# Kernel tuning notes

Measured on AMD Instinct MI355X. Metric: run time of the kernel, lower is better.

The kernel has to match this reference:

```python
import jax, jax.numpy as jnp
import numpy as np

B, T, C, H = 4, 2048, 1024, 16
D = C // H  # head dim = 64


def setup_inputs() -> dict:
    key = jax.random.key(0)
    ks = jax.random.split(key, 5)
    s = 1.0 / np.sqrt(C)
    return {
        "x": jax.random.normal(ks[0], (B, T, C), dtype=jnp.float32),
        "Wq": jax.random.normal(ks[1], (C, C), dtype=jnp.float32) * s,
        "bq": jnp.zeros((C,), dtype=jnp.float32),
        "Wk": jax.random.normal(ks[2], (C, C), dtype=jnp.float32) * s,
        "bk": jnp.zeros((C,), dtype=jnp.float32),
        "Wv": jax.random.normal(ks[3], (C, C), dtype=jnp.float32) * s,
        "bv": jnp.zeros((C,), dtype=jnp.float32),
        "Wp": jax.random.normal(ks[4], (C, C), dtype=jnp.float32) * s,
        "bp": jnp.zeros((C,), dtype=jnp.float32),
    }


def reference(x, Wq, bq, Wk, bk, Wv, bv, Wp, bp):
    Bb, Tt, Cc = x.shape
    # QKV projections (torch Linear: y = x @ W.T + b)
    q = (x @ Wq.T + bq).reshape(Bb, Tt, H, D).transpose(0, 2, 1, 3)  # [B,H,T,D]
    k = (x @ Wk.T + bk).reshape(Bb, Tt, H, D).transpose(0, 2, 1, 3)
    v = (x @ Wv.T + bv).reshape(Bb, Tt, H, D).transpose(0, 2, 1, 3)
    att = jnp.einsum("bhqd,bhkd->bhqk", q, k) / jnp.sqrt(jnp.float32(D))
    causal = jnp.tril(jnp.ones((Tt, Tt), dtype=bool))
    att = jnp.where(causal[None, None], att, -jnp.inf)
    att = jax.nn.softmax(att, axis=-1)
    y = jnp.einsum("bhqk,bhkd->bhqd", att, v)  # [B,H,T,D]
    y = y.transpose(0, 2, 1, 3).reshape(Bb, Tt, Cc)
    return y @ Wp.T + bp
```

## Files before the change

### kernel.cpp

```cpp
#include <hip/hip_runtime.h>

typedef unsigned short u16;
typedef unsigned int u32;

typedef __attribute__((ext_vector_type(4))) float f32x4;
typedef __attribute__((ext_vector_type(8))) short bf16x8;


__device__ inline u16 f2b(float f) {
  union { float f; u32 u; } x; x.f = f;
  u32 u = x.u;
  u32 r = (u + 0x7fffu + ((u >> 16) & 1u)) >> 16;
  return (u16)r;
}

__device__ inline u32 cvtpk(float lo, float hi) {
  u32 r;
  asm("v_cvt_pk_bf16_f32 %0, %1, %2" : "=v"(r) : "v"(lo), "v"(hi));
  return r;
}

__device__ inline void gload_lds16(const void* g, void* l) {
  __builtin_amdgcn_global_load_lds(
      (const __attribute__((address_space(1))) u32*)g,
      (__attribute__((address_space(3))) u32*)l, 16, 0, 0);
}


__global__ __launch_bounds__(256) void cvt_all(const float* __restrict__ x,
                                               const float* __restrict__ w0,
                                               const float* __restrict__ w1,
                                               const float* __restrict__ w2,
                                               const float* __restrict__ w3,
                                               u16* __restrict__ xs,
                                               u16* __restrict__ wsz,
                                               u16* __restrict__ wp) {
  int b = blockIdx.x, t = threadIdx.x;
  const float* src;
  char* dst;
  if (b < 5632) {
    int g = b * 256 + t;
    int row;
    if (b < 4096) {
      row = g >> 7;
      src = x + (size_t)row * 1024;
      dst = (char*)xs;
    } else {
      g -= 1048576;
      row = g >> 7;
      src = (row < 1024) ? w0 + (size_t)row * 1024
           : (row < 2048) ? w1 + (size_t)(row - 1024) * 1024
                          : w2 + (size_t)(row - 2048) * 1024;
      dst = (char*)wsz;
    }
    int c = g & 127;
    int kt = c >> 3, cc = (c & 7) ^ (row & 7);
    float4 lo = *(const float4*)(src + c * 8);
    float4 hi = *(const float4*)(src + c * 8 + 4);
    union { u16 s[8]; uint4 v; } o;
    o.s[0] = f2b(lo.x); o.s[1] = f2b(lo.y); o.s[2] = f2b(lo.z); o.s[3] = f2b(lo.w);
    o.s[4] = f2b(hi.x); o.s[5] = f2b(hi.y); o.s[6] = f2b(hi.z); o.s[7] = f2b(hi.w);
    *(uint4*)(dst + (size_t)(row >> 8) * 524288 + kt * 32768 +
              (row & 255) * 128 + cc * 16) = o.v;
  } else {
    int g = (b - 5632) * 256 + t;
    float4 lo = *(const float4*)(w3 + (size_t)g * 8);
    float4 hi = *(const float4*)(w3 + (size_t)g * 8 + 4);
    union { u16 s[8]; uint4 v; } o;
    o.s[0] = f2b(lo.x); o.s[1] = f2b(lo.y); o.s[2] = f2b(lo.z); o.s[3] = f2b(lo.w);
    o.s[4] = f2b(hi.x); o.s[5] = f2b(hi.y); o.s[6] = f2b(hi.z); o.s[7] = f2b(hi.w);
    *(uint4*)((char*)wp + (size_t)g * 16) = o.v;
  }
}


__global__ __launch_bounds__(512) void gemm_qkv(const u16* __restrict__ Aswz,
                                                const u16* __restrict__ Wswz,
                                                const float* __restrict__ bq,
                                                const float* __restrict__ bk,
                                                const float* __restrict__ bv,
                                                u16* __restrict__ outQ,
                                                u16* __restrict__ outK,
                                                u16* __restrict__ outVt,
                                                float qscale) {
  __shared__ u16 lds[3][24576];

  const int t = threadIdx.x;
  const int lane = t & 63;
  const int w = t >> 6;
  const int wm = w >> 1, wn = w & 1;
  const int lr = lane & 15, lg = lane >> 4;

  int bid = blockIdx.y * 24 + blockIdx.x;
  int swz = (bid & 7) * 96 + (bid >> 3);
  const int mBase = (swz / 24) * 256;
  const int nBase = (swz % 24) * 128;
  const int mode = nBase >> 10;
  const int noff = nBase & 255;

  const char* Ap = (const char*)Aswz + (size_t)(mBase >> 8) * 524288;
  const char* Bp = (const char*)Wswz + (size_t)(nBase >> 8) * 524288 +
                   noff * 128;

  f32x4 acc[4][4];
#pragma unroll
  for (int i = 0; i < 4; ++i)
#pragma unroll
    for (int j = 0; j < 4; ++j) acc[i][j] = (f32x4){0.f, 0.f, 0.f, 0.f};

  auto stage = [&](int buf, int kt2) {
    const char* As = Ap + (size_t)kt2 * 32768;
    const char* Bs = Bp + (size_t)kt2 * 32768;
    char* Ad = (char*)&lds[buf][0];
    char* Bd = (char*)&lds[buf][16384];
#pragma unroll
    for (int l = 0; l < 4; ++l)
      gload_lds16(As + (l * 512 + t) * 16, Ad + (l * 512 + t) * 16);
#pragma unroll
    for (int l = 0; l < 2; ++l)
      gload_lds16(Bs + (l * 512 + t) * 16, Bd + (l * 512 + t) * 16);
  };

  stage(0, 0);
  stage(1, 1);

  for (int kt = 0; kt < 16; ++kt) {
    if (kt < 15) asm volatile("s_waitcnt vmcnt(6)" ::: "memory");
    else         asm volatile("s_waitcnt vmcnt(0)" ::: "memory");
    __builtin_amdgcn_s_barrier();
    if (kt + 2 < 16) stage((kt + 2) % 3, kt + 2);

    const int cb = kt % 3;
    const char* Ab = (const char*)&lds[cb][0];
    const char* Bb = (const char*)&lds[cb][16384];

    bf16x8 af[4][2], bf[4][2];
#pragma unroll
    for (int i = 0; i < 4; ++i) {
      int row = wm * 64 + i * 16 + lr;
#pragma unroll
      for (int kk = 0; kk < 2; ++kk)
        af[i][kk] = *(const bf16x8*)(Ab + row * 128 +
                                     ((kk * 64 + lg * 16) ^ ((row & 7) << 4)));
    }
#pragma unroll
    for (int j = 0; j < 4; ++j) {
      int rn = wn * 64 + j * 16 + lr;
#pragma unroll
      for (int kk = 0; kk < 2; ++kk)
        bf[j][kk] = *(const bf16x8*)(Bb + rn * 128 +
                                     ((kk * 64 + lg * 16) ^ ((rn & 7) << 4)));
    }

    __builtin_amdgcn_s_setprio(1);
#pragma unroll
    for (int i = 0; i < 4; ++i)
#pragma unroll
      for (int j = 0; j < 4; ++j)
#pragma unroll
        for (int kk = 0; kk < 2; ++kk)
          acc[i][j] = __builtin_amdgcn_mfma_f32_16x16x32_bf16(
              af[i][kk], bf[j][kk], acc[i][j], 0, 0, 0);
    __builtin_amdgcn_s_setprio(0);
  }

#pragma unroll
  for (int i = 0; i < 4; ++i) {
    int row = mBase + wm * 64 + i * 16 + lg * 4;
    int b_ = row >> 11, tp = row & 2047;
#pragma unroll
    for (int j = 0; j < 4; ++j) {
      int col = nBase + wn * 64 + j * 16 + lr;
      int ncol = col & 1023;
      int h = ncol >> 6, dd = ncol & 63;
      size_t bhOff = (size_t)(b_ * 16 + h) * 262144;
      if (mode == 2) {
        float bv_ = bv[ncol];
        ushort4 o;
        o.x = f2b(acc[i][j][0] + bv_);
        o.y = f2b(acc[i][j][1] + bv_);
        o.z = f2b(acc[i][j][2] + bv_);
        o.w = f2b(acc[i][j][3] + bv_);
        *(ushort4*)((char*)outVt + bhOff + (tp >> 6) * 8192 + dd * 128 +
                    ((((tp & 63) >> 3) << 4) ^ ((dd & 7) << 4)) +
                    (tp & 7) * 2) = o;
      } else if (mode == 0) {
        float bv_ = bq[ncol];
#pragma unroll
        for (int r = 0; r < 4; ++r)
          outQ[(((size_t)(b_ * 16 + h) * 2048) + tp + r) * 64 + dd] =
              f2b((acc[i][j][r] + bv_) * qscale);
      } else {
        float bv_ = bk[ncol];
#pragma unroll
        for (int r = 0; r < 4; ++r) {
          int tt = tp + r;
          *(u16*)((char*)outK + bhOff + (tt >> 6) * 8192 + (tt & 63) * 128 +
                  (((dd >> 3) << 4) ^ ((tt & 7) << 4)) + (dd & 7) * 2) =
              f2b(acc[i][j][r] + bv_);
        }
      }
    }
  }
}


__global__ __launch_bounds__(256) void gemm_proj(const u16* __restrict__ A,
                                                 const u16* __restrict__ W,
                                                 const float* __restrict__ bias,
                                                 float* __restrict__ outF) {
  __shared__ u16 sA[8192];
  __shared__ u16 sB[8192];

  const int K = 1024, N = 1024;
  const int t = threadIdx.x;
  const int lane = t & 63;
  const int w = t >> 6;
  const int wr = w >> 1, wc = w & 1;
  const int lr = lane & 15, lg = lane >> 4;

  int bid = blockIdx.y * 8 + blockIdx.x;
  int swz = (bid & 7) * 64 + (bid >> 3);
  const int mBase = (swz >> 3) * 128;
  const int nBase = (swz & 7) * 128;

  f32x4 zero = {0.f, 0.f, 0.f, 0.f};
  f32x4 acc[4][4];
#pragma unroll
  for (int i = 0; i < 4; ++i)
#pragma unroll
    for (int j = 0; j < 4; ++j) acc[i][j] = zero;

  const int rA = t >> 2;
  const int cA = (t & 3) * 8;

  for (int k0 = 0; k0 < K; k0 += 64) {
#pragma unroll
    for (int hh = 0; hh < 2; ++hh)
#pragma unroll
      for (int i = 0; i < 2; ++i) {
        gload_lds16(A + (size_t)(mBase + i * 64 + rA) * K + k0 + hh * 32 + cA,
                    &sA[hh * 4096 + i * 2048 + t * 8]);
        gload_lds16(W + (size_t)(nBase + i * 64 + rA) * K + k0 + hh * 32 + cA,
                    &sB[hh * 4096 + i * 2048 + t * 8]);
      }
    __syncthreads();

#pragma unroll
    for (int hh = 0; hh < 2; ++hh) {
      bf16x8 af[4], bf[4];
#pragma unroll
      for (int i = 0; i < 4; ++i)
        af[i] = *(const bf16x8*)&sA[hh * 4096 +
                                    (wr * 64 + i * 16 + lr) * 32 + lg * 8];
#pragma unroll
      for (int j = 0; j < 4; ++j)
        bf[j] = *(const bf16x8*)&sB[hh * 4096 +
                                    (wc * 64 + j * 16 + lr) * 32 + lg * 8];

#pragma unroll
      for (int i = 0; i < 4; ++i)
#pragma unroll
        for (int j = 0; j < 4; ++j)
          acc[i][j] = __builtin_amdgcn_mfma_f32_16x16x32_bf16(af[i], bf[j],
                                                              acc[i][j], 0, 0, 0);
    }
    __syncthreads();
  }

#pragma unroll
  for (int i = 0; i < 4; ++i) {
    int row = mBase + wr * 64 + i * 16 + lg * 4;
#pragma unroll
    for (int j = 0; j < 4; ++j) {
      int col = nBase + wc * 64 + j * 16 + lr;
      float bv = bias[col];
#pragma unroll
      for (int r = 0; r < 4; ++r)
        outF[(size_t)(row + r) * N + col] = acc[i][j][r] + bv;
    }
  }
}


__global__ __launch_bounds__(512) void attn_fwd(const u16* __restrict__ qg,
                                                const u16* __restrict__ kswz,
                                                const u16* __restrict__ vswz,
                                                u16* __restrict__ yg) {
  __shared__ u16 sK[2][64 * 64];
  __shared__ u16 sVt[2][64 * 64];

  const int t = threadIdx.x;
  const int lane = t & 63;
  const int w = t >> 6;
  const int lr = lane & 15, lg = lane >> 4;
  const int xk = (lr & 7) << 4;

  int bid0 = blockIdx.y * 8 + blockIdx.x;
  int swzb = (bid0 & 7) * 64 + (bid0 >> 3);
  const int bh = swzb >> 3;
  const int pair = swzb & 7;

  const char* kgb = (const char*)kswz + (size_t)bh * 262144;
  const char* vgb = (const char*)vswz + (size_t)bh * 262144;
  const u16* qb = qg + (size_t)bh * 131072;

  gload_lds16(kgb + t * 16, (char*)&sK[0][0] + t * 16);
  gload_lds16(vgb + t * 16, (char*)&sVt[0][0] + t * 16);

  f32x4 zero = {0.f, 0.f, 0.f, 0.f};
  const int b = bh >> 4, h = bh & 15;
  int tc = 0;

  for (int half = 0; half < 2; ++half) {
    const int qt = half ? pair : 15 - pair;
    const int nkt = 2 * qt + 2;
    const int wq0 = qt * 128 + w * 16;
    const int qrow = wq0 + lr;

    bf16x8 qf[2];
#pragma unroll
    for (int kk = 0; kk < 2; ++kk)
      qf[kk] = *(const bf16x8*)(qb + (size_t)qrow * 64 + kk * 32 + lg * 8);

    f32x4 accO[4];
#pragma unroll
    for (int n = 0; n < 4; ++n) accO[n] = zero;
    float lrun = 0.f;

    for (int kt = 0; kt < nkt; ++kt, ++tc) {
      const int cur = tc & 1;
      __syncthreads();

      int nextT = (kt + 1 < nkt) ? kt + 1 : (half == 0 ? 0 : -1);
      if (nextT >= 0) {
        gload_lds16(kgb + nextT * 8192 + t * 16,
                    (char*)&sK[cur ^ 1][0] + t * 16);
        gload_lds16(vgb + nextT * 8192 + t * 16,
                    (char*)&sVt[cur ^ 1][0] + t * 16);
      }

      if (kt * 64 > wq0 + 15) continue;

      const char* kb_ = (const char*)&sK[cur][0];
      const char* vb_ = (const char*)&sVt[cur][0];

      f32x4 s[4];
      __builtin_amdgcn_s_setprio(1);
#pragma unroll
      for (int n = 0; n < 4; ++n) {
        f32x4 a = zero;
#pragma unroll
        for (int kk = 0; kk < 2; ++kk) {
          bf16x8 kf = *(const bf16x8*)(kb_ + (n * 16 + lr) * 128 +
                                       ((kk * 64 + lg * 16) ^ xk));
          a = __builtin_amdgcn_mfma_f32_16x16x32_bf16(kf, qf[kk], a, 0, 0, 0);
        }
        s[n] = a;
      }
      __builtin_amdgcn_s_setprio(0);

      if (kt * 64 + 63 > wq0) {
#pragma unroll
        for (int n = 0; n < 4; ++n) {
          int key0 = kt * 64 + n * 16 + lg * 4;
#pragma unroll
          for (int r = 0; r < 4; ++r)
            s[n][r] = (key0 + r <= qrow) ? s[n][r] : -1e30f;
        }
      }

      u32 pk[4][2];
#pragma unroll
      for (int n = 0; n < 4; ++n) {
        float p0 = exp2f(s[n][0] - 12.f);
        float p1 = exp2f(s[n][1] - 12.f);
        float p2 = exp2f(s[n][2] - 12.f);
        float p3 = exp2f(s[n][3] - 12.f);
        lrun += (p0 + p1) + (p2 + p3);
        pk[n][0] = cvtpk(p0, p1);
        pk[n][1] = cvtpk(p2, p3);
      }

      const bool hi = (lg >> 1) & 1;
#pragma unroll
      for (int kk = 0; kk < 2; ++kk) {
        u32 g[4];
#pragma unroll
        for (int r = 0; r < 4; ++r) {
          const int rh = r >> 1, rl = r & 1;
          u32 give = ((lg & 1) ^ rh) ? pk[2 * kk + 1][rl] : pk[2 * kk][rl];
          int srcLane = ((lg & 1) * 2 + ((lg >> 1) ^ rh)) * 16 + lr;
          g[r] = (u32)__shfl((int)give, srcLane);
        }
        union { u32 u[4]; bf16x8 v; } pu;
        pu.u[0] = hi ? g[2] : g[0];
        pu.u[1] = hi ? g[3] : g[1];
        pu.u[2] = hi ? g[0] : g[2];
        pu.u[3] = hi ? g[1] : g[3];
        bf16x8 pf = pu.v;
        __builtin_amdgcn_s_setprio(1);
#pragma unroll
        for (int n = 0; n < 4; ++n) {
          bf16x8 vf = *(const bf16x8*)(vb_ + (n * 16 + lr) * 128 +
                                       ((kk * 64 + lg * 16) ^ xk));
          accO[n] = __builtin_amdgcn_mfma_f32_16x16x32_bf16(pf, vf, accO[n], 0, 0, 0);
        }
        __builtin_amdgcn_s_setprio(0);
      }
    }

    lrun += __shfl_xor(lrun, 16);
    lrun += __shfl_xor(lrun, 32);

#pragma unroll
    for (int r = 0; r < 4; ++r) {
      float linv = 1.f / __shfl(lrun, lg * 4 + r);
      int trow = qt * 128 + w * 16 + lg * 4 + r;
      size_t rowOff = ((size_t)b * 2048 + trow) * 1024 + h * 64;
#pragma unroll
      for (int n = 0; n < 4; ++n)
        yg[rowOff + n * 16 + lr] = f2b(accO[n][r] * linv);
    }
  }
}


extern "C" void kernel_launch(void* const* d_in, const int* in_sizes, int n_in,
                              void* d_out, int out_size, void* d_ws, size_t ws_size,
                              hipStream_t stream) {
  const float* x  = (const float*)d_in[0];
  const float* Wq = (const float*)d_in[1];
  const float* bq = (const float*)d_in[2];
  const float* Wk = (const float*)d_in[3];
  const float* bk = (const float*)d_in[4];
  const float* Wv = (const float*)d_in[5];
  const float* bv = (const float*)d_in[6];
  const float* Wp = (const float*)d_in[7];
  const float* bp = (const float*)d_in[8];
  float* out = (float*)d_out;

  char* ws = (char*)d_ws;
  u16* xb  = (u16*)(ws);
  u16* wqb = (u16*)(ws + (16u << 20));
  u16* wpb = (u16*)(ws + (22u << 20));
  u16* qb  = (u16*)(ws + (24u << 20));
  u16* kb  = (u16*)(ws + (40u << 20));
  u16* vtb = (u16*)(ws + (56u << 20));
  u16* yb  = (u16*)(ws + (72u << 20));

  const float SCL = 0.18033688011112042f;

  cvt_all<<<6144, 256, 0, stream>>>(x, Wq, Wk, Wv, Wp, xb, wqb, wpb);

  gemm_qkv<<<dim3(24, 32), 512, 0, stream>>>(xb, wqb, bq, bk, bv,
                                             qb, kb, vtb, SCL);

  attn_fwd<<<dim3(8, 64), 512, 0, stream>>>(qb, kb, vtb, yb);

  gemm_proj<<<dim3(8, 64), 256, 0, stream>>>(yb, wpb, bp, out);
}
```

Baseline: 184.0 us.

## Triple-buffer K/V tiles in attention with two-ahead async prefetch

Grows the K and V shared-memory staging from two to three buffers and issues global-to-LDS loads two tiles ahead over a flattened tile index that spans both query halves. The __syncthreads is replaced by an explicit vmcnt wait plus s_barrier, so only the oldest outstanding load pair must finish before compute. The aim is to hide more global-load latency behind the MFMA work. In exchange it uses more LDS, which could reduce occupancy, and relies on correct hand-placed waitcnt ordering.

```diff
diff --git a/kernel.cpp b/kernel.cpp
--- a/kernel.cpp
+++ b/kernel.cpp
@@ -287,8 +287,8 @@
                                                 const u16* __restrict__ kswz,
                                                 const u16* __restrict__ vswz,
                                                 u16* __restrict__ yg) {
-  __shared__ u16 sK[2][64 * 64];
-  __shared__ u16 sVt[2][64 * 64];
+  __shared__ u16 sK[3][64 * 64];
+  __shared__ u16 sVt[3][64 * 64];
 
   const int t = threadIdx.x;
   const int lane = t & 63;
@@ -305,15 +305,25 @@
   const char* vgb = (const char*)vswz + (size_t)bh * 262144;
   const u16* qb = qg + (size_t)bh * 131072;
 
-  gload_lds16(kgb + t * 16, (char*)&sK[0][0] + t * 16);
-  gload_lds16(vgb + t * 16, (char*)&sVt[0][0] + t * 16);
+  const int qt0 = 15 - pair;
+  const int n0 = 2 * qt0 + 2;
+  const int ntot = 34;
+
+  auto goff = [&](int g) -> int {
+    return (g < n0) ? g * 8192 : ((g < ntot) ? (g - n0) * 8192 : -1);
+  };
+
+  gload_lds16(kgb + goff(0) + t * 16, (char*)&sK[0][0] + t * 16);
+  gload_lds16(vgb + goff(0) + t * 16, (char*)&sVt[0][0] + t * 16);
+  gload_lds16(kgb + goff(1) + t * 16, (char*)&sK[1][0] + t * 16);
+  gload_lds16(vgb + goff(1) + t * 16, (char*)&sVt[1][0] + t * 16);
 
   f32x4 zero = {0.f, 0.f, 0.f, 0.f};
   const int b = bh >> 4, h = bh & 15;
   int tc = 0;
 
   for (int half = 0; half < 2; ++half) {
-    const int qt = half ? pair : 15 - pair;
+    const int qt = half ? pair : qt0;
     const int nkt = 2 * qt + 2;
     const int wq0 = qt * 128 + w * 16;
     const int qrow = wq0 + lr;
@@ -329,21 +339,21 @@
     float lrun = 0.f;
 
     for (int kt = 0; kt < nkt; ++kt, ++tc) {
-      const int cur = tc & 1;
-      __syncthreads();
-
-      int nextT = (kt + 1 < nkt) ? kt + 1 : (half == 0 ? 0 : -1);
-      if (nextT >= 0) {
-        gload_lds16(kgb + nextT * 8192 + t * 16,
-                    (char*)&sK[cur ^ 1][0] + t * 16);
-        gload_lds16(vgb + nextT * 8192 + t * 16,
-                    (char*)&sVt[cur ^ 1][0] + t * 16);
+      if (tc + 1 < ntot) asm volatile("s_waitcnt vmcnt(2)" ::: "memory");
+      else               asm volatile("s_waitcnt vmcnt(0)" ::: "memory");
+      __builtin_amdgcn_s_barrier();
+
+      int o2 = goff(tc + 2);
+      if (o2 >= 0) {
+        int nb = (tc + 2) % 3;
+        gload_lds16(kgb + o2 + t * 16, (char*)&sK[nb][0] + t * 16);
+        gload_lds16(vgb + o2 + t * 16, (char*)&sVt[nb][0] + t * 16);
       }
 
       if (kt * 64 > wq0 + 15) continue;
 
-      const char* kb_ = (const char*)&sK[cur][0];
-      const char* vb_ = (const char*)&sVt[cur][0];
+      const char* kb_ = (const char*)&sK[tc % 3][0];
+      const char* vb_ = (const char*)&sVt[tc % 3][0];
 
       f32x4 s[4];
       __builtin_amdgcn_s_setprio(1);
```

Result: no change. 185.7 us (+0.9%).

## Rewrite projection GEMM with swizzled panel layout and triple-buffered pipelining

Applied to the files above, without the earlier changes.

The output projection GEMM now uses the same swizzled k-panel layout as the QKV GEMM. Attention writes its output directly in that layout, and the Wp conversion produces it too. The new gemm_proj uses 512 threads, 256x128 tiles and a three-stage LDS ring driven by direct global-to-LDS loads and vmcnt waits, so loads overlap compute instead of syncing every K step. The cost is larger LDS use per block, fewer blocks (256), and scattered 2-byte stores in the attention epilogue.

```diff
diff --git a/kernel.cpp b/kernel.cpp
--- a/kernel.cpp
+++ b/kernel.cpp
@@ -34,43 +34,36 @@
                                                const float* __restrict__ w3,
                                                u16* __restrict__ xs,
                                                u16* __restrict__ wsz,
-                                               u16* __restrict__ wp) {
-  int b = blockIdx.x, t = threadIdx.x;
+                                               u16* __restrict__ wps) {
+  int g = blockIdx.x * 256 + threadIdx.x;
+  int grow = g >> 7;
+  int c = g & 127;
   const float* src;
   char* dst;
-  if (b < 5632) {
-    int g = b * 256 + t;
-    int row;
-    if (b < 4096) {
-      row = g >> 7;
-      src = x + (size_t)row * 1024;
-      dst = (char*)xs;
-    } else {
-      g -= 1048576;
-      row = g >> 7;
-      src = (row < 1024) ? w0 + (size_t)row * 1024
-           : (row < 2048) ? w1 + (size_t)(row - 1024) * 1024
-                          : w2 + (size_t)(row - 2048) * 1024;
-      dst = (char*)wsz;
-    }
-    int c = g & 127;
-    int kt = c >> 3, cc = (c & 7) ^ (row & 7);
-    float4 lo = *(const float4*)(src + c * 8);
-    float4 hi = *(const float4*)(src + c * 8 + 4);
-    union { u16 s[8]; uint4 v; } o;
-    o.s[0] = f2b(lo.x); o.s[1] = f2b(lo.y); o.s[2] = f2b(lo.z); o.s[3] = f2b(lo.w);
-    o.s[4] = f2b(hi.x); o.s[5] = f2b(hi.y); o.s[6] = f2b(hi.z); o.s[7] = f2b(hi.w);
-    *(uint4*)(dst + (size_t)(row >> 8) * 524288 + kt * 32768 +
-              (row & 255) * 128 + cc * 16) = o.v;
+  int row;
+  if (grow < 8192) {
+    row = grow;
+    src = x + (size_t)row * 1024;
+    dst = (char*)xs;
+  } else if (grow < 11264) {
+    row = grow - 8192;
+    src = (row < 1024) ? w0 + (size_t)row * 1024
+         : (row < 2048) ? w1 + (size_t)(row - 1024) * 1024
+                        : w2 + (size_t)(row - 2048) * 1024;
+    dst = (char*)wsz;
   } else {
-    int g = (b - 5632) * 256 + t;
-    float4 lo = *(const float4*)(w3 + (size_t)g * 8);
-    float4 hi = *(const float4*)(w3 + (size_t)g * 8 + 4);
-    union { u16 s[8]; uint4 v; } o;
-    o.s[0] = f2b(lo.x); o.s[1] = f2b(lo.y); o.s[2] = f2b(lo.z); o.s[3] = f2b(lo.w);
-    o.s[4] = f2b(hi.x); o.s[5] = f2b(hi.y); o.s[6] = f2b(hi.z); o.s[7] = f2b(hi.w);
-    *(uint4*)((char*)wp + (size_t)g * 16) = o.v;
-  }
+    row = grow - 11264;
+    src = w3 + (size_t)row * 1024;
+    dst = (char*)wps;
+  }
+  int kt = c >> 3, cc = (c & 7) ^ (row & 7);
+  float4 lo = *(const float4*)(src + c * 8);
+  float4 hi = *(const float4*)(src + c * 8 + 4);
+  union { u16 s[8]; uint4 v; } o;
+  o.s[0] = f2b(lo.x); o.s[1] = f2b(lo.y); o.s[2] = f2b(lo.z); o.s[3] = f2b(lo.w);
+  o.s[4] = f2b(hi.x); o.s[5] = f2b(hi.y); o.s[6] = f2b(hi.z); o.s[7] = f2b(hi.w);
+  *(uint4*)(dst + (size_t)(row >> 8) * 524288 + kt * 32768 +
+            (row & 255) * 128 + cc * 16) = o.v;
 }
 
 
@@ -205,79 +198,99 @@
 }
 
 
-__global__ __launch_bounds__(256) void gemm_proj(const u16* __restrict__ A,
-                                                 const u16* __restrict__ W,
+__global__ __launch_bounds__(512) void gemm_proj(const u16* __restrict__ Aswz,
+                                                 const u16* __restrict__ Wswz,
                                                  const float* __restrict__ bias,
                                                  float* __restrict__ outF) {
-  __shared__ u16 sA[8192];
-  __shared__ u16 sB[8192];
-
-  const int K = 1024, N = 1024;
+  __shared__ u16 lds[3][24576];
+
   const int t = threadIdx.x;
   const int lane = t & 63;
   const int w = t >> 6;
-  const int wr = w >> 1, wc = w & 1;
+  const int wm = w >> 1, wn = w & 1;
   const int lr = lane & 15, lg = lane >> 4;
 
   int bid = blockIdx.y * 8 + blockIdx.x;
-  int swz = (bid & 7) * 64 + (bid >> 3);
-  const int mBase = (swz >> 3) * 128;
+  int swz = (bid & 7) * 32 + (bid >> 3);
+  const int mBase = (swz >> 3) * 256;
   const int nBase = (swz & 7) * 128;
 
-  f32x4 zero = {0.f, 0.f, 0.f, 0.f};
+  const char* Ap = (const char*)Aswz + (size_t)(mBase >> 8) * 524288;
+  const char* Bp = (const char*)Wswz + (size_t)(nBase >> 8) * 524288 +
+                   (nBase & 255) * 128;
+
   f32x4 acc[4][4];
 #pragma unroll
   for (int i = 0; i < 4; ++i)
 #pragma unroll
-    for (int j = 0; j < 4; ++j) acc[i][j] = zero;
-
-  const int rA = t >> 2;
-  const int cA = (t & 3) * 8;
-
-  for (int k0 = 0; k0 < K; k0 += 64) {
-#pragma unroll
-    for (int hh = 0; hh < 2; ++hh)
-#pragma unroll
-      for (int i = 0; i < 2; ++i) {
-        gload_lds16(A + (size_t)(mBase + i * 64 + rA) * K + k0 + hh * 32 + cA,
-                    &sA[hh * 4096 + i * 2048 + t * 8]);
-        gload_lds16(W + (size_t)(nBase + i * 64 + rA) * K + k0 + hh * 32 + cA,
-                    &sB[hh * 4096 + i * 2048 + t * 8]);
-      }
-    __syncthreads();
-
-#pragma unroll
-    for (int hh = 0; hh < 2; ++hh) {
-      bf16x8 af[4], bf[4];
-#pragma unroll
-      for (int i = 0; i < 4; ++i)
-        af[i] = *(const bf16x8*)&sA[hh * 4096 +
-                                    (wr * 64 + i * 16 + lr) * 32 + lg * 8];
+    for (int j = 0; j < 4; ++j) acc[i][j] = (f32x4){0.f, 0.f, 0.f, 0.f};
+
+  auto stage = [&](int buf, int kt2) {
+    const char* As = Ap + (size_t)kt2 * 32768;
+    const char* Bs = Bp + (size_t)kt2 * 32768;
+    char* Ad = (char*)&lds[buf][0];
+    char* Bd = (char*)&lds[buf][16384];
+#pragma unroll
+    for (int l = 0; l < 4; ++l)
+      gload_lds16(As + (l * 512 + t) * 16, Ad + (l * 512 + t) * 16);
+#pragma unroll
+    for (int l = 0; l < 2; ++l)
+      gload_lds16(Bs + (l * 512 + t) * 16, Bd + (l * 512 + t) * 16);
+  };
+
+  stage(0, 0);
+  stage(1, 1);
+
+  for (int kt = 0; kt < 16; ++kt) {
+    if (kt < 15) asm volatile("s_waitcnt vmcnt(6)" ::: "memory");
+    else         asm volatile("s_waitcnt vmcnt(0)" ::: "memory");
+    __builtin_amdgcn_s_barrier();
+    if (kt + 2 < 16) stage((kt + 2) % 3, kt + 2);
+
+    const int cb = kt % 3;
+    const char* Ab = (const char*)&lds[cb][0];
+    const char* Bb = (const char*)&lds[cb][16384];
+
+    bf16x8 af[4][2], bf[4][2];
+#pragma unroll
+    for (int i = 0; i < 4; ++i) {
+      int row = wm * 64 + i * 16 + lr;
+#pragma unroll
+      for (int kk = 0; kk < 2; ++kk)
+        af[i][kk] = *(const bf16x8*)(Ab + row * 128 +
+                                     ((kk * 64 + lg * 16) ^ ((row & 7) << 4)));
+    }
+#pragma unroll
+    for (int j = 0; j < 4; ++j) {
+      int rn = wn * 64 + j * 16 + lr;
+#pragma unroll
+      for (int kk = 0; kk < 2; ++kk)
+        bf[j][kk] = *(const bf16x8*)(Bb + rn * 128 +
+                                     ((kk * 64 + lg * 16) ^ ((rn & 7) << 4)));
+    }
+
+    __builtin_amdgcn_s_setprio(1);
+#pragma unroll
+    for (int i = 0; i < 4; ++i)
 #pragma unroll
       for (int j = 0; j < 4; ++j)
-        bf[j] = *(const bf16x8*)&sB[hh * 4096 +
-                                    (wc * 64 + j * 16 + lr) * 32 + lg * 8];
-
-#pragma unroll
-      for (int i = 0; i < 4; ++i)
-#pragma unroll
-        for (int j = 0; j < 4; ++j)
-          acc[i][j] = __builtin_amdgcn_mfma_f32_16x16x32_bf16(af[i], bf[j],
-                                                              acc[i][j], 0, 0, 0);
-    }
-    __syncthreads();
+#pragma unroll
+        for (int kk = 0; kk < 2; ++kk)
+          acc[i][j] = __builtin_amdgcn_mfma_f32_16x16x32_bf16(
+              af[i][kk], bf[j][kk], acc[i][j], 0, 0, 0);
+    __builtin_amdgcn_s_setprio(0);
   }
 
 #pragma unroll
   for (int i = 0; i < 4; ++i) {
-    int row = mBase + wr * 64 + i * 16 + lg * 4;
+    int row = mBase + wm * 64 + i * 16 + lg * 4;
 #pragma unroll
     for (int j = 0; j < 4; ++j) {
-      int col = nBase + wc * 64 + j * 16 + lr;
+      int col = nBase + wn * 64 + j * 16 + lr;
       float bv = bias[col];
 #pragma unroll
       for (int r = 0; r < 4; ++r)
-        outF[(size_t)(row + r) * N + col] = acc[i][j][r] + bv;
+        outF[(size_t)(row + r) * 1024 + col] = acc[i][j][r] + bv;
     }
   }
 }
@@ -286,7 +299,7 @@
 __global__ __launch_bounds__(512) void attn_fwd(const u16* __restrict__ qg,
                                                 const u16* __restrict__ kswz,
                                                 const u16* __restrict__ vswz,
-                                                u16* __restrict__ yg) {
+                                                u16* __restrict__ ypan) {
   __shared__ u16 sK[2][64 * 64];
   __shared__ u16 sVt[2][64 * 64];
 
@@ -416,11 +429,15 @@
 #pragma unroll
     for (int r = 0; r < 4; ++r) {
       float linv = 1.f / __shfl(lrun, lg * 4 + r);
-      int trow = qt * 128 + w * 16 + lg * 4 + r;
-      size_t rowOff = ((size_t)b * 2048 + trow) * 1024 + h * 64;
-#pragma unroll
-      for (int n = 0; n < 4; ++n)
-        yg[rowOff + n * 16 + lr] = f2b(accO[n][r] * linv);
+      int row = b * 2048 + qt * 128 + w * 16 + lg * 4 + r;
+      char* rp = (char*)ypan + (size_t)(row >> 8) * 524288 +
+                 h * 32768 + (row & 255) * 128;
+#pragma unroll
+      for (int n = 0; n < 4; ++n) {
+        int cl = n * 16 + lr;
+        *(u16*)(rp + ((((cl >> 3) ^ (row & 7)) << 4)) + (cl & 7) * 2) =
+            f2b(accO[n][r] * linv);
+      }
     }
   }
 }
@@ -458,5 +475,5 @@
 
   attn_fwd<<<dim3(8, 64), 512, 0, stream>>>(qb, kb, vtb, yb);
 
-  gemm_proj<<<dim3(8, 64), 256, 0, stream>>>(yb, wpb, bp, out);
-}
+  gemm_proj<<<dim3(8, 32), 512, 0, stream>>>(yb, wpb, bp, out);
+}
```

Result: faster. 175.9 us (median of 3 runs) (-4.4%).
